# Optimization experiments

Measured on AMD Instinct MI355X. Metric: run time of the kernel, lower is better.

The kernel has to match this reference:

```python
import jax, jax.numpy as jnp
import numpy as np

D_MODEL = 1024
NHEAD = 16
D_FF = 4096
LN_EPS = 1e-5


def _layer_norm(x, g, b):
    mu = jnp.mean(x, axis=-1, keepdims=True)
    var = jnp.mean(jnp.square(x - mu), axis=-1, keepdims=True)
    return (x - mu) * jax.lax.rsqrt(var + LN_EPS) * g + b


def setup_inputs() -> dict:
    key = jax.random.key(0)
    ks = jax.random.split(key, 12)
    d, f = D_MODEL, D_FF
    s = 1.0 / np.sqrt(d)
    inp = {
        "src": jax.random.normal(ks[0], (2, 2048, d), dtype=jnp.float32),
        "Wq": jax.random.uniform(ks[1], (d, d), jnp.float32, -s, s),
        "bq": jnp.zeros((d,), jnp.float32),
        "Wk": jax.random.uniform(ks[2], (d, d), jnp.float32, -s, s),
        "bk": jnp.zeros((d,), jnp.float32),
        "Wv": jax.random.uniform(ks[3], (d, d), jnp.float32, -s, s),
        "bv": jnp.zeros((d,), jnp.float32),
        "Wo": jax.random.uniform(ks[4], (d, d), jnp.float32, -s, s),
        "bo": jnp.zeros((d,), jnp.float32),
        "W1": jax.random.uniform(ks[5], (d, f), jnp.float32, -s, s),
        "b1": jnp.zeros((f,), jnp.float32),
        "W2": jax.random.uniform(ks[6], (f, d), jnp.float32, -1.0 / np.sqrt(f), 1.0 / np.sqrt(f)),
        "b2": jnp.zeros((d,), jnp.float32),
        "ln1_g": jnp.ones((d,), jnp.float32),
        "ln1_b": jnp.zeros((d,), jnp.float32),
        "ln2_g": jnp.ones((d,), jnp.float32),
        "ln2_b": jnp.zeros((d,), jnp.float32),
    }
    return inp


def reference(src, Wq, bq, Wk, bk, Wv, bv, Wo, bo, W1, b1, W2, b2,
              ln1_g, ln1_b, ln2_g, ln2_b):
    B, S, D = src.shape
    H = NHEAD
    hd = D // H
    # QKV projections, split into heads: [B, H, S, hd]
    q = (src @ Wq + bq).reshape(B, S, H, hd).transpose(0, 2, 1, 3)
    k = (src @ Wk + bk).reshape(B, S, H, hd).transpose(0, 2, 1, 3)
    v = (src @ Wv + bv).reshape(B, S, H, hd).transpose(0, 2, 1, 3)
    # Explicit full-score attention (no mask branch), as in source.
    scores = jnp.einsum("bhqd,bhkd->bhqk", q, k) / jnp.sqrt(jnp.asarray(hd, src.dtype))
    attn = jax.nn.softmax(scores, axis=-1)
    ctx = jnp.einsum("bhqk,bhkd->bhqd", attn, v)
    ctx = ctx.transpose(0, 2, 1, 3).reshape(B, S, D)
    src2 = ctx @ Wo + bo
    x = _layer_norm(src + src2, ln1_g, ln1_b)
    ff = jax.nn.relu(x @ W1 + b1) @ W2 + b2
    out = _layer_norm(x + ff, ln2_g, ln2_b)
    return out
```

## Files before the change

kernel.cpp:

```cpp
#include <hip/hip_runtime.h>
#include <cstdint>
#include <cstddef>

#define SEQ 2048
#define BATCH 2
#define ROWS (BATCH * SEQ)

typedef __attribute__((ext_vector_type(8))) short short8;
typedef __attribute__((ext_vector_type(4))) float f32x4;
typedef __attribute__((ext_vector_type(8))) _Float16 half8;
typedef __attribute__((ext_vector_type(2))) __fp16 fp16x2;

__device__ __forceinline__ unsigned short f2bf(float f) {
  union { float f; uint32_t u; } v; v.f = f;
  uint32_t r = v.u + 0x7fffu + ((v.u >> 16) & 1u);
  return (unsigned short)(r >> 16);
}

__device__ __forceinline__ unsigned short bf2h(unsigned short b) {
  union { uint32_t u; float f; } v; v.u = ((uint32_t)b) << 16;
  union { _Float16 h; unsigned short u; } o; o.h = (_Float16)v.f;
  return o.u;
}

__device__ __forceinline__ void async16(const void* g, void* l) {
  __builtin_amdgcn_global_load_lds((const __attribute__((address_space(1))) void*)g,
                                   (__attribute__((address_space(3))) void*)l, 16, 0, 0);
}

__global__ __launch_bounds__(256) void f2bf_kernel(const float* __restrict__ in,
                                                   unsigned short* __restrict__ out) {
  size_t i = ((size_t)blockIdx.x * 256 + threadIdx.x) * 4;
  float4 vv = *(const float4*)(in + i);
  ushort4 o;
  o.x = f2bf(vv.x); o.y = f2bf(vv.y); o.z = f2bf(vv.z); o.w = f2bf(vv.w);
  *(ushort4*)(out + i) = o;
}

__global__ __launch_bounds__(256) void wtrans(const float* __restrict__ W,
                                              unsigned short* __restrict__ WT,
                                              int K, int N, float scale) {
  __shared__ float t[32][33];
  int n0 = blockIdx.x * 32, k0 = blockIdx.y * 32;
  for (int i = threadIdx.y; i < 32; i += 8)
    t[i][threadIdx.x] = W[(size_t)(k0 + i) * N + n0 + threadIdx.x];
  __syncthreads();
  for (int i = threadIdx.y; i < 32; i += 8)
    WT[(size_t)(n0 + i) * K + k0 + threadIdx.x] = f2bf(t[threadIdx.x][i] * scale);
}

__global__ __launch_bounds__(256) void bias_concat(const float* __restrict__ bq,
                                                   const float* __restrict__ bk,
                                                   const float* __restrict__ bv,
                                                   float* __restrict__ o) {
  int i = blockIdx.x * 256 + threadIdx.x;
  float v = (i < 1024) ? bq[i] * 0.18033688f : (i < 2048 ? bk[i - 1024] : bv[i - 2048]);
  o[i] = v;
}

__global__ __launch_bounds__(256) void vtrans(const unsigned short* __restrict__ qkv,
                                              unsigned short* __restrict__ VT) {
  const int st = blockIdx.x, bh = blockIdx.y, b = bh >> 4, h = bh & 15;
  __shared__ unsigned short t[64][72];
  const int tid = threadIdx.x;
#pragma unroll
  for (int it = 0; it < 2; ++it) {
    int i = it * 256 + tid;
    int s = i >> 3, c = (i & 7) * 8;
    short8 v = *(const short8*)(qkv + ((size_t)b * SEQ + st * 64 + s) * 3072 + 2048 + h * 64 + c);
#pragma unroll
    for (int j = 0; j < 8; ++j) t[c + j][s] = bf2h((unsigned short)v[j]);
  }
  __syncthreads();
#pragma unroll
  for (int it = 0; it < 2; ++it) {
    int i = it * 256 + tid;
    int d = i >> 3, sc = (i & 7) * 8;
    short8 o;
#pragma unroll
    for (int j = 0; j < 8; ++j) o[j] = (short)t[d][sc + j];
    *(short8*)(VT + ((size_t)bh * 64 + d) * 2048 + st * 64 + sc) = o;
  }
}

template <bool RELU, bool OUTBF, bool HASRES>
__global__ __launch_bounds__(256) void gemm_bt(
    const unsigned short* __restrict__ A, const unsigned short* __restrict__ BT,
    const float* __restrict__ bias, const float* __restrict__ Rres,
    float* __restrict__ outF, unsigned short* __restrict__ outB,
    int M, int N, int K) {
  __shared__ unsigned short As[2][128 * 32];
  __shared__ unsigned short Bs[2][128 * 32];
  const int tid = threadIdx.x;
  const int lane = tid & 63, ln = lane & 15, quad = lane >> 4;
  const int w = tid >> 6;
  const int m0 = blockIdx.y * 128, n0 = blockIdx.x * 128;
  const int mw = (w >> 1) * 64, nw = (w & 1) * 64;
  f32x4 acc[4][4] = {};
  const int i0 = tid, i1 = tid + 256;
  const int r0 = i0 >> 2, kc0 = (i0 & 3) * 8;
  const int r1 = i1 >> 2, kc1 = (i1 & 3) * 8;
  for (int k0 = 0; k0 < K; k0 += 64) {
    __syncthreads();
#pragma unroll
    for (int p = 0; p < 2; ++p) {
      const int kp = k0 + p * 32;
      async16(A + (size_t)(m0 + r0) * K + kp + kc0, &As[p][i0 * 8]);
      async16(A + (size_t)(m0 + r1) * K + kp + kc1, &As[p][i1 * 8]);
      async16(BT + (size_t)(n0 + r0) * K + kp + kc0, &Bs[p][i0 * 8]);
      async16(BT + (size_t)(n0 + r1) * K + kp + kc1, &Bs[p][i1 * 8]);
    }
    __syncthreads();
#pragma unroll
    for (int p = 0; p < 2; ++p) {
      short8 a[4], b[4];
#pragma unroll
      for (int mi = 0; mi < 4; ++mi)
        a[mi] = *(const short8*)&As[p][(mw + mi * 16 + ln) * 32 + quad * 8];
#pragma unroll
      for (int ni = 0; ni < 4; ++ni)
        b[ni] = *(const short8*)&Bs[p][(nw + ni * 16 + ln) * 32 + quad * 8];
#pragma unroll
      for (int mi = 0; mi < 4; ++mi)
#pragma unroll
        for (int ni = 0; ni < 4; ++ni)
          acc[mi][ni] = __builtin_amdgcn_mfma_f32_16x16x32_bf16(a[mi], b[ni], acc[mi][ni], 0, 0, 0);
    }
  }
#pragma unroll
  for (int mi = 0; mi < 4; ++mi) {
#pragma unroll
    for (int ni = 0; ni < 4; ++ni) {
#pragma unroll
      for (int reg = 0; reg < 4; ++reg) {
        int row = m0 + mw + mi * 16 + quad * 4 + reg;
        int col = n0 + nw + ni * 16 + ln;
        float v = acc[mi][ni][reg] + bias[col];
        if (HASRES) v += Rres[(size_t)row * N + col];
        if (RELU) v = fmaxf(v, 0.f);
        if (OUTBF) outB[(size_t)row * N + col] = f2bf(v);
        else outF[(size_t)row * N + col] = v;
      }
    }
  }
}

template <bool RELU, bool OUTBF, bool HASRES>
__global__ __launch_bounds__(256) void gemm_bt64(
    const unsigned short* __restrict__ A, const unsigned short* __restrict__ BT,
    const float* __restrict__ bias, const float* __restrict__ Rres,
    float* __restrict__ outF, unsigned short* __restrict__ outB,
    int M, int N, int K) {
  __shared__ unsigned short As[4][128 * 32];
  __shared__ unsigned short Bs[4][64 * 32];
  const int tid = threadIdx.x;
  const int lane = tid & 63, ln = lane & 15, quad = lane >> 4;
  const int w = tid >> 6;
  const int m0 = blockIdx.y * 128, n0 = blockIdx.x * 64;
  const int mw = w * 32;
  f32x4 acc[2][4] = {};
  const int i0 = tid, i1 = tid + 256;
  const int r0 = i0 >> 2, kc0 = (i0 & 3) * 8;
  const int r1 = i1 >> 2, kc1 = (i1 & 3) * 8;
  for (int k0 = 0; k0 < K; k0 += 128) {
    __syncthreads();
#pragma unroll
    for (int p = 0; p < 4; ++p) {
      const int kp = k0 + p * 32;
      async16(A + (size_t)(m0 + r0) * K + kp + kc0, &As[p][i0 * 8]);
      async16(A + (size_t)(m0 + r1) * K + kp + kc1, &As[p][i1 * 8]);
      async16(BT + (size_t)(n0 + r0) * K + kp + kc0, &Bs[p][i0 * 8]);
    }
    __syncthreads();
#pragma unroll
    for (int p = 0; p < 4; ++p) {
      short8 a[2], b[4];
#pragma unroll
      for (int mi = 0; mi < 2; ++mi)
        a[mi] = *(const short8*)&As[p][(mw + mi * 16 + ln) * 32 + quad * 8];
#pragma unroll
      for (int ni = 0; ni < 4; ++ni)
        b[ni] = *(const short8*)&Bs[p][(ni * 16 + ln) * 32 + quad * 8];
#pragma unroll
      for (int mi = 0; mi < 2; ++mi)
#pragma unroll
        for (int ni = 0; ni < 4; ++ni)
          acc[mi][ni] = __builtin_amdgcn_mfma_f32_16x16x32_bf16(a[mi], b[ni], acc[mi][ni], 0, 0, 0);
    }
  }
#pragma unroll
  for (int mi = 0; mi < 2; ++mi) {
#pragma unroll
    for (int ni = 0; ni < 4; ++ni) {
#pragma unroll
      for (int reg = 0; reg < 4; ++reg) {
        int row = m0 + mw + mi * 16 + quad * 4 + reg;
        int col = n0 + ni * 16 + ln;
        float v = acc[mi][ni][reg] + bias[col];
        if (HASRES) v += Rres[(size_t)row * N + col];
        if (RELU) v = fmaxf(v, 0.f);
        if (OUTBF) outB[(size_t)row * N + col] = f2bf(v);
        else outF[(size_t)row * N + col] = v;
      }
    }
  }
}

__global__ __launch_bounds__(256) void attn_kernel(const unsigned short* __restrict__ qkv,
                                                   const unsigned short* __restrict__ VT,
                                                   unsigned short* __restrict__ ctx) {
  const int qt = blockIdx.x;
  const int bh = blockIdx.y, b = bh >> 4, h = bh & 15;
  const int tid = threadIdx.x;
  const int w = tid >> 6, lane = tid & 63, ln = lane & 15, quad = lane >> 4;
  __shared__ __align__(16) unsigned short Qs[4096];
  __shared__ __align__(16) unsigned short Ks[4096];
  __shared__ __align__(16) unsigned short Vs[4096];
  __shared__ __align__(16) unsigned short Ps[4096];
  const size_t rowbase = (size_t)b * SEQ;
  const unsigned short* kbase = qkv + (rowbase)*3072 + 1024 + h * 64;
  const unsigned short* vbase = VT + (size_t)bh * 64 * 2048;
  const int r0 = tid >> 3, c0 = tid & 7;
  const int r1 = r0 + 32;
  const int sw0 = r0 * 64 + ((c0 ^ (r0 & 7)) * 8);
  const int sw1 = r1 * 64 + ((c0 ^ (r1 & 7)) * 8);
  {
    const unsigned short* qb = qkv + (rowbase + qt * 64) * 3072 + h * 64;
    *(short8*)&Qs[sw0] = *(const short8*)(qb + (size_t)r0 * 3072 + c0 * 8);
    *(short8*)&Qs[sw1] = *(const short8*)(qb + (size_t)r1 * 3072 + c0 * 8);
  }
  short8 kreg0 = *(const short8*)(kbase + (size_t)r0 * 3072 + c0 * 8);
  short8 kreg1 = *(const short8*)(kbase + (size_t)r1 * 3072 + c0 * 8);
  short8 vreg0 = *(const short8*)(vbase + (size_t)r0 * 2048 + c0 * 8);
  short8 vreg1 = *(const short8*)(vbase + (size_t)r1 * 2048 + c0 * 8);
  *(short8*)&Ks[sw0] = kreg0;
  *(short8*)&Ks[sw1] = kreg1;
  *(short8*)&Vs[sw0] = vreg0;
  *(short8*)&Vs[sw1] = vreg1;
  __syncthreads();
  const int lh = ln & 7;
  short8 aq0 = *(const short8*)&Qs[(w * 16 + ln) * 64 + ((0 + quad) ^ lh) * 8];
  short8 aq1 = *(const short8*)&Qs[(w * 16 + ln) * 64 + ((4 + quad) ^ lh) * 8];
  f32x4 oacc[4] = {};
  float lsum[4] = {0.f, 0.f, 0.f, 0.f};
  unsigned short* Pw = &Ps[w * 1024];
  const int pr0 = ln * 64 + ((0 + quad) ^ lh) * 8;
  const int pr1 = ln * 64 + ((4 + quad) ^ lh) * 8;
  for (int kt = 0; kt < 32; ++kt) {
    if (kt < 31) {
      const unsigned short* kp = kbase + (size_t)(kt + 1) * 64 * 3072;
      const unsigned short* vp = vbase + (kt + 1) * 64;
      kreg0 = *(const short8*)(kp + (size_t)r0 * 3072 + c0 * 8);
      kreg1 = *(const short8*)(kp + (size_t)r1 * 3072 + c0 * 8);
      vreg0 = *(const short8*)(vp + (size_t)r0 * 2048 + c0 * 8);
      vreg1 = *(const short8*)(vp + (size_t)r1 * 2048 + c0 * 8);
    }
#pragma unroll
    for (int nt = 0; nt < 4; ++nt) {
      short8 bk0 = *(const short8*)&Ks[(nt * 16 + ln) * 64 + ((0 + quad) ^ lh) * 8];
      short8 bk1 = *(const short8*)&Ks[(nt * 16 + ln) * 64 + ((4 + quad) ^ lh) * 8];
      f32x4 z = {};
      z = __builtin_amdgcn_mfma_f32_16x16x32_bf16(aq0, bk0, z, 0, 0, 0);
      z = __builtin_amdgcn_mfma_f32_16x16x32_bf16(aq1, bk1, z, 0, 0, 0);
      const int pc = nt * 2 + (ln >> 3);
      float p0 = __builtin_amdgcn_exp2f(z[0]);
      float p1 = __builtin_amdgcn_exp2f(z[1]);
      float p2 = __builtin_amdgcn_exp2f(z[2]);
      float p3 = __builtin_amdgcn_exp2f(z[3]);
      lsum[0] += p0; lsum[1] += p1; lsum[2] += p2; lsum[3] += p3;
      union { fp16x2 h; unsigned short u[2]; } ca, cb;
      ca.h = __builtin_amdgcn_cvt_pkrtz(p0, p1);
      cb.h = __builtin_amdgcn_cvt_pkrtz(p2, p3);
      const int q4 = quad * 4;
      Pw[(q4 + 0) * 64 + ((pc ^ ((q4 + 0) & 7)) * 8) + lh] = ca.u[0];
      Pw[(q4 + 1) * 64 + ((pc ^ ((q4 + 1) & 7)) * 8) + lh] = ca.u[1];
      Pw[(q4 + 2) * 64 + ((pc ^ ((q4 + 2) & 7)) * 8) + lh] = cb.u[0];
      Pw[(q4 + 3) * 64 + ((pc ^ ((q4 + 3) & 7)) * 8) + lh] = cb.u[1];
    }
    asm volatile("s_waitcnt lgkmcnt(0)" ::: "memory");
    half8 ap0 = *(const half8*)&Pw[pr0];
    half8 ap1 = *(const half8*)&Pw[pr1];
#pragma unroll
    for (int ot = 0; ot < 4; ++ot) {
      half8 bv0 = *(const half8*)&Vs[(ot * 16 + ln) * 64 + ((0 + quad) ^ lh) * 8];
      half8 bv1 = *(const half8*)&Vs[(ot * 16 + ln) * 64 + ((4 + quad) ^ lh) * 8];
      oacc[ot] = __builtin_amdgcn_mfma_f32_16x16x32_f16(ap0, bv0, oacc[ot], 0, 0, 0);
      oacc[ot] = __builtin_amdgcn_mfma_f32_16x16x32_f16(ap1, bv1, oacc[ot], 0, 0, 0);
    }
    if (kt < 31) {
      __syncthreads();
      *(short8*)&Ks[sw0] = kreg0;
      *(short8*)&Ks[sw1] = kreg1;
      *(short8*)&Vs[sw0] = vreg0;
      *(short8*)&Vs[sw1] = vreg1;
      __syncthreads();
    }
  }
  float rl[4];
#pragma unroll
  for (int r = 0; r < 4; ++r) {
    float l = lsum[r];
#pragma unroll
    for (int off = 1; off < 16; off <<= 1) l += __shfl_xor(l, off);
    rl[r] = 1.0f / l;
  }
#pragma unroll
  for (int ot = 0; ot < 4; ++ot)
#pragma unroll
    for (int r = 0; r < 4; ++r) {
      int s = qt * 64 + w * 16 + quad * 4 + r;
      int c = h * 64 + ot * 16 + ln;
      ctx[(rowbase + s) * 1024 + c] = f2bf(oacc[ot][r] * rl[r]);
    }
}

__global__ __launch_bounds__(256) void ln_kernel(const float* __restrict__ y,
                                                 const float* __restrict__ g,
                                                 const float* __restrict__ bb,
                                                 float* __restrict__ outF,
                                                 unsigned short* __restrict__ outB) {
  const int row = blockIdx.x;
  const int tid = threadIdx.x;
  const float* yr = y + (size_t)row * 1024;
  float v[4]; float s = 0.f, s2 = 0.f;
#pragma unroll
  for (int j = 0; j < 4; ++j) {
    v[j] = yr[tid + j * 256];
    s += v[j]; s2 += v[j] * v[j];
  }
#pragma unroll
  for (int off = 1; off < 64; off <<= 1) {
    s += __shfl_xor(s, off);
    s2 += __shfl_xor(s2, off);
  }
  __shared__ float ws1[4], ws2[4];
  if ((tid & 63) == 0) { ws1[tid >> 6] = s; ws2[tid >> 6] = s2; }
  __syncthreads();
  s = ws1[0] + ws1[1] + ws1[2] + ws1[3];
  s2 = ws2[0] + ws2[1] + ws2[2] + ws2[3];
  const float mu = s * (1.f / 1024.f);
  const float var = s2 * (1.f / 1024.f) - mu * mu;
  const float rstd = rsqrtf(var + 1e-5f);
#pragma unroll
  for (int j = 0; j < 4; ++j) {
    int c = tid + j * 256;
    float val = (v[j] - mu) * rstd * g[c] + bb[c];
    if (outF) outF[(size_t)row * 1024 + c] = val;
    if (outB) outB[(size_t)row * 1024 + c] = f2bf(val);
  }
}

extern "C" void kernel_launch(void* const* d_in, const int* in_sizes, int n_in,
                              void* d_out, int out_size, void* d_ws, size_t ws_size,
                              hipStream_t stream) {
  const float* src = (const float*)d_in[0];
  const float* Wq = (const float*)d_in[1];
  const float* bq = (const float*)d_in[2];
  const float* Wk = (const float*)d_in[3];
  const float* bk = (const float*)d_in[4];
  const float* Wv = (const float*)d_in[5];
  const float* bv = (const float*)d_in[6];
  const float* Wo = (const float*)d_in[7];
  const float* bo = (const float*)d_in[8];
  const float* W1 = (const float*)d_in[9];
  const float* b1 = (const float*)d_in[10];
  const float* W2 = (const float*)d_in[11];
  const float* b2 = (const float*)d_in[12];
  const float* ln1g = (const float*)d_in[13];
  const float* ln1b = (const float*)d_in[14];
  const float* ln2g = (const float*)d_in[15];
  const float* ln2b = (const float*)d_in[16];
  float* out = (float*)d_out;

  char* ws = (char*)d_ws;
  unsigned short* qkvT = (unsigned short*)(ws + 0);
  unsigned short* WoT  = (unsigned short*)(ws + 6291456);
  unsigned short* W1T  = (unsigned short*)(ws + 8388608);
  unsigned short* W2T  = (unsigned short*)(ws + 16777216);
  float*          biasq = (float*)(ws + 25165824);
  unsigned short* xbf  = (unsigned short*)(ws + 25178112);
  unsigned short* qkv  = (unsigned short*)(ws + 33566720);
  unsigned short* hbuf = qkv;
  unsigned short* ctx  = (unsigned short*)(ws + 58732544);
  float*          ybuf = (float*)(ws + 67121152);
  unsigned short* VT   = (unsigned short*)(ws + 67121152);
  float*          xf   = (float*)(ws + 83898368);

  const float QSCALE = 0.18033688f;

  f2bf_kernel<<<4096, 256, 0, stream>>>(src, xbf);
  wtrans<<<dim3(32, 32), dim3(32, 8), 0, stream>>>(Wq, qkvT, 1024, 1024, QSCALE);
  wtrans<<<dim3(32, 32), dim3(32, 8), 0, stream>>>(Wk, qkvT + 1024 * 1024, 1024, 1024, 1.0f);
  wtrans<<<dim3(32, 32), dim3(32, 8), 0, stream>>>(Wv, qkvT + 2048 * 1024, 1024, 1024, 1.0f);
  wtrans<<<dim3(32, 32), dim3(32, 8), 0, stream>>>(Wo, WoT, 1024, 1024, 1.0f);
  wtrans<<<dim3(128, 32), dim3(32, 8), 0, stream>>>(W1, W1T, 1024, 4096, 1.0f);
  wtrans<<<dim3(32, 128), dim3(32, 8), 0, stream>>>(W2, W2T, 4096, 1024, 1.0f);
  bias_concat<<<12, 256, 0, stream>>>(bq, bk, bv, biasq);

  gemm_bt<false, true, false><<<dim3(24, 32), 256, 0, stream>>>(
      xbf, qkvT, biasq, nullptr, nullptr, qkv, ROWS, 3072, 1024);
  vtrans<<<dim3(32, 32), 256, 0, stream>>>(qkv, VT);
  attn_kernel<<<dim3(32, 32), 256, 0, stream>>>(qkv, VT, ctx);
  gemm_bt64<false, false, true><<<dim3(16, 32), 256, 0, stream>>>(
      ctx, WoT, bo, src, ybuf, nullptr, ROWS, 1024, 1024);
  ln_kernel<<<4096, 256, 0, stream>>>(ybuf, ln1g, ln1b, xf, xbf);
  gemm_bt<true, true, false><<<dim3(32, 32), 256, 0, stream>>>(
      xbf, W1T, b1, nullptr, nullptr, hbuf, ROWS, 4096, 1024);
  gemm_bt64<false, false, true><<<dim3(16, 32), 256, 0, stream>>>(
      hbuf, W2T, b2, xf, ybuf, nullptr, ROWS, 1024, 4096);
  ln_kernel<<<4096, 256, 0, stream>>>(ybuf, ln2g, ln2b, out, nullptr);
}
```

Before: 401.7 us.

## Process 128 query rows per attention block to reuse K/V tiles

```diff
diff --git a/kernel.cpp b/kernel.cpp
--- a/kernel.cpp
+++ b/kernel.cpp
@@ -213,10 +213,10 @@
   const int bh = blockIdx.y, b = bh >> 4, h = bh & 15;
   const int tid = threadIdx.x;
   const int w = tid >> 6, lane = tid & 63, ln = lane & 15, quad = lane >> 4;
-  __shared__ __align__(16) unsigned short Qs[4096];
+  __shared__ __align__(16) unsigned short Qs[8192];
   __shared__ __align__(16) unsigned short Ks[4096];
   __shared__ __align__(16) unsigned short Vs[4096];
-  __shared__ __align__(16) unsigned short Ps[4096];
+  __shared__ __align__(16) unsigned short Ps[8192];
   const size_t rowbase = (size_t)b * SEQ;
   const unsigned short* kbase = qkv + (rowbase)*3072 + 1024 + h * 64;
   const unsigned short* vbase = VT + (size_t)bh * 64 * 2048;
@@ -225,9 +225,14 @@
   const int sw0 = r0 * 64 + ((c0 ^ (r0 & 7)) * 8);
   const int sw1 = r1 * 64 + ((c0 ^ (r1 & 7)) * 8);
   {
-    const unsigned short* qb = qkv + (rowbase + qt * 64) * 3072 + h * 64;
-    *(short8*)&Qs[sw0] = *(const short8*)(qb + (size_t)r0 * 3072 + c0 * 8);
-    *(short8*)&Qs[sw1] = *(const short8*)(qb + (size_t)r1 * 3072 + c0 * 8);
+    const unsigned short* qb = qkv + (rowbase + qt * 128) * 3072 + h * 64;
+#pragma unroll
+    for (int it = 0; it < 4; ++it) {
+      int i = it * 256 + tid;
+      int r = i >> 3, c = (i & 7) * 8;
+      *(short8*)&Qs[r * 64 + (((i & 7) ^ (r & 7)) * 8)] =
+          *(const short8*)(qb + (size_t)r * 3072 + c);
+    }
   }
   short8 kreg0 = *(const short8*)(kbase + (size_t)r0 * 3072 + c0 * 8);
   short8 kreg1 = *(const short8*)(kbase + (size_t)r1 * 3072 + c0 * 8);
@@ -239,11 +244,15 @@
   *(short8*)&Vs[sw1] = vreg1;
   __syncthreads();
   const int lh = ln & 7;
-  short8 aq0 = *(const short8*)&Qs[(w * 16 + ln) * 64 + ((0 + quad) ^ lh) * 8];
-  short8 aq1 = *(const short8*)&Qs[(w * 16 + ln) * 64 + ((4 + quad) ^ lh) * 8];
-  f32x4 oacc[4] = {};
-  float lsum[4] = {0.f, 0.f, 0.f, 0.f};
-  unsigned short* Pw = &Ps[w * 1024];
+  short8 aq[2][2];
+#pragma unroll
+  for (int s = 0; s < 2; ++s) {
+    const int qrow = s * 64 + w * 16 + ln;
+    aq[s][0] = *(const short8*)&Qs[qrow * 64 + ((0 + quad) ^ lh) * 8];
+    aq[s][1] = *(const short8*)&Qs[qrow * 64 + ((4 + quad) ^ lh) * 8];
+  }
+  f32x4 oacc[2][4] = {};
+  float lsum[2][4] = {};
   const int pr0 = ln * 64 + ((0 + quad) ^ lh) * 8;
   const int pr1 = ln * 64 + ((4 + quad) ^ lh) * 8;
   for (int kt = 0; kt < 32; ++kt) {
@@ -256,36 +265,44 @@
       vreg1 = *(const short8*)(vp + (size_t)r1 * 2048 + c0 * 8);
     }
 #pragma unroll
-    for (int nt = 0; nt < 4; ++nt) {
-      short8 bk0 = *(const short8*)&Ks[(nt * 16 + ln) * 64 + ((0 + quad) ^ lh) * 8];
-      short8 bk1 = *(const short8*)&Ks[(nt * 16 + ln) * 64 + ((4 + quad) ^ lh) * 8];
-      f32x4 z = {};
-      z = __builtin_amdgcn_mfma_f32_16x16x32_bf16(aq0, bk0, z, 0, 0, 0);
-      z = __builtin_amdgcn_mfma_f32_16x16x32_bf16(aq1, bk1, z, 0, 0, 0);
-      const int pc = nt * 2 + (ln >> 3);
-      float p0 = __builtin_amdgcn_exp2f(z[0]);
-      float p1 = __builtin_amdgcn_exp2f(z[1]);
-      float p2 = __builtin_amdgcn_exp2f(z[2]);
-      float p3 = __builtin_amdgcn_exp2f(z[3]);
-      lsum[0] += p0; lsum[1] += p1; lsum[2] += p2; lsum[3] += p3;
-      union { fp16x2 h; unsigned short u[2]; } ca, cb;
-      ca.h = __builtin_amdgcn_cvt_pkrtz(p0, p1);
-      cb.h = __builtin_amdgcn_cvt_pkrtz(p2, p3);
-      const int q4 = quad * 4;
-      Pw[(q4 + 0) * 64 + ((pc ^ ((q4 + 0) & 7)) * 8) + lh] = ca.u[0];
-      Pw[(q4 + 1) * 64 + ((pc ^ ((q4 + 1) & 7)) * 8) + lh] = ca.u[1];
-      Pw[(q4 + 2) * 64 + ((pc ^ ((q4 + 2) & 7)) * 8) + lh] = cb.u[0];
-      Pw[(q4 + 3) * 64 + ((pc ^ ((q4 + 3) & 7)) * 8) + lh] = cb.u[1];
+    for (int s = 0; s < 2; ++s) {
+      unsigned short* Pw = &Ps[(w * 2 + s) * 1024];
+#pragma unroll
+      for (int nt = 0; nt < 4; ++nt) {
+        short8 bk0 = *(const short8*)&Ks[(nt * 16 + ln) * 64 + ((0 + quad) ^ lh) * 8];
+        short8 bk1 = *(const short8*)&Ks[(nt * 16 + ln) * 64 + ((4 + quad) ^ lh) * 8];
+        f32x4 z = {};
+        z = __builtin_amdgcn_mfma_f32_16x16x32_bf16(aq[s][0], bk0, z, 0, 0, 0);
+        z = __builtin_amdgcn_mfma_f32_16x16x32_bf16(aq[s][1], bk1, z, 0, 0, 0);
+        const int pc = nt * 2 + (ln >> 3);
+        float p0 = __builtin_amdgcn_exp2f(z[0]);
+        float p1 = __builtin_amdgcn_exp2f(z[1]);
+        float p2 = __builtin_amdgcn_exp2f(z[2]);
+        float p3 = __builtin_amdgcn_exp2f(z[3]);
+        lsum[s][0] += p0; lsum[s][1] += p1; lsum[s][2] += p2; lsum[s][3] += p3;
+        union { fp16x2 h; unsigned short u[2]; } ca, cb;
+        ca.h = __builtin_amdgcn_cvt_pkrtz(p0, p1);
+        cb.h = __builtin_amdgcn_cvt_pkrtz(p2, p3);
+        const int q4 = quad * 4;
+        Pw[(q4 + 0) * 64 + ((pc ^ ((q4 + 0) & 7)) * 8) + lh] = ca.u[0];
+        Pw[(q4 + 1) * 64 + ((pc ^ ((q4 + 1) & 7)) * 8) + lh] = ca.u[1];
+        Pw[(q4 + 2) * 64 + ((pc ^ ((q4 + 2) & 7)) * 8) + lh] = cb.u[0];
+        Pw[(q4 + 3) * 64 + ((pc ^ ((q4 + 3) & 7)) * 8) + lh] = cb.u[1];
+      }
     }
     asm volatile("s_waitcnt lgkmcnt(0)" ::: "memory");
-    half8 ap0 = *(const half8*)&Pw[pr0];
-    half8 ap1 = *(const half8*)&Pw[pr1];
-#pragma unroll
-    for (int ot = 0; ot < 4; ++ot) {
-      half8 bv0 = *(const half8*)&Vs[(ot * 16 + ln) * 64 + ((0 + quad) ^ lh) * 8];
-      half8 bv1 = *(const half8*)&Vs[(ot * 16 + ln) * 64 + ((4 + quad) ^ lh) * 8];
-      oacc[ot] = __builtin_amdgcn_mfma_f32_16x16x32_f16(ap0, bv0, oacc[ot], 0, 0, 0);
-      oacc[ot] = __builtin_amdgcn_mfma_f32_16x16x32_f16(ap1, bv1, oacc[ot], 0, 0, 0);
+#pragma unroll
+    for (int s = 0; s < 2; ++s) {
+      const unsigned short* Pw = &Ps[(w * 2 + s) * 1024];
+      half8 ap0 = *(const half8*)&Pw[pr0];
+      half8 ap1 = *(const half8*)&Pw[pr1];
+#pragma unroll
+      for (int ot = 0; ot < 4; ++ot) {
+        half8 bv0 = *(const half8*)&Vs[(ot * 16 + ln) * 64 + ((0 + quad) ^ lh) * 8];
+        half8 bv1 = *(const half8*)&Vs[(ot * 16 + ln) * 64 + ((4 + quad) ^ lh) * 8];
+        oacc[s][ot] = __builtin_amdgcn_mfma_f32_16x16x32_f16(ap0, bv0, oacc[s][ot], 0, 0, 0);
+        oacc[s][ot] = __builtin_amdgcn_mfma_f32_16x16x32_f16(ap1, bv1, oacc[s][ot], 0, 0, 0);
+      }
     }
     if (kt < 31) {
       __syncthreads();
@@ -296,22 +313,25 @@
       __syncthreads();
     }
   }
-  float rl[4];
-#pragma unroll
-  for (int r = 0; r < 4; ++r) {
-    float l = lsum[r];
-#pragma unroll
-    for (int off = 1; off < 16; off <<= 1) l += __shfl_xor(l, off);
-    rl[r] = 1.0f / l;
-  }
-#pragma unroll
-  for (int ot = 0; ot < 4; ++ot)
+#pragma unroll
+  for (int s = 0; s < 2; ++s) {
+    float rl[4];
 #pragma unroll
     for (int r = 0; r < 4; ++r) {
-      int s = qt * 64 + w * 16 + quad * 4 + r;
-      int c = h * 64 + ot * 16 + ln;
-      ctx[(rowbase + s) * 1024 + c] = f2bf(oacc[ot][r] * rl[r]);
-    }
+      float l = lsum[s][r];
+#pragma unroll
+      for (int off = 1; off < 16; off <<= 1) l += __shfl_xor(l, off);
+      rl[r] = 1.0f / l;
+    }
+#pragma unroll
+    for (int ot = 0; ot < 4; ++ot)
+#pragma unroll
+      for (int r = 0; r < 4; ++r) {
+        int srow = qt * 128 + s * 64 + w * 16 + quad * 4 + r;
+        int c = h * 64 + ot * 16 + ln;
+        ctx[(rowbase + srow) * 1024 + c] = f2bf(oacc[s][ot][r] * rl[r]);
+      }
+  }
 }
 
 __global__ __launch_bounds__(256) void ln_kernel(const float* __restrict__ y,
@@ -400,7 +420,7 @@
   gemm_bt<false, true, false><<<dim3(24, 32), 256, 0, stream>>>(
       xbf, qkvT, biasq, nullptr, nullptr, qkv, ROWS, 3072, 1024);
   vtrans<<<dim3(32, 32), 256, 0, stream>>>(qkv, VT);
-  attn_kernel<<<dim3(32, 32), 256, 0, stream>>>(qkv, VT, ctx);
+  attn_kernel<<<dim3(16, 32), 256, 0, stream>>>(qkv, VT, ctx);
   gemm_bt64<false, false, true><<<dim3(16, 32), 256, 0, stream>>>(
       ctx, WoT, bo, src, ybuf, nullptr, ROWS, 1024, 1024);
   ln_kernel<<<4096, 256, 0, stream>>>(ybuf, ln1g, ln1b, xf, xbf);
```

Result: no change. 402.9 us (+0.3%).
